# Optimization experiments

Measured on AMD Instinct MI355X. Metric: run time of the kernel, lower is better.

The kernel has to match this reference:

```python
import jax, jax.numpy as jnp
import numpy as np

NEG_SLOPE = 0.2
EPS = 1e-16


def gat_conv(x, src, dst, n_nodes, W, att_src, att_dst, b):
    """PyG GATConv, heads=1. x:[N,in], W:[out,in], att_*:[out], b:[out].
    Messages flow src->dst; softmax over incoming edges of each dst node."""
    h = x @ W.T                                  # [N, out]
    a_src = h @ att_src                          # [N]
    a_dst = h @ att_dst                          # [N]
    e = jax.nn.leaky_relu(a_src[src] + a_dst[dst], NEG_SLOPE)   # [E]
    m = jax.ops.segment_max(e, dst, num_segments=n_nodes)       # [N]
    ex = jnp.exp(e - m[dst])                                    # [E]
    denom = jax.ops.segment_sum(ex, dst, num_segments=n_nodes)  # [N]
    alpha = ex / (denom[dst] + EPS)                             # [E]
    out = jax.ops.segment_sum(h[src] * alpha[:, None], dst, num_segments=n_nodes)
    return out + b


def setup_inputs() -> dict:
    key = jax.random.key(0)
    ks = jax.random.split(key, 12)
    N, E = 100000, 1280000
    d_in, d_hid, d_out = 2, 64, 2

    def glorot(k, shape):
        fan = shape[-1] + shape[0]
        s = jnp.sqrt(6.0 / fan)
        return jax.random.uniform(k, shape, jnp.float32, -s, s)

    return {
        "x": jax.random.normal(ks[0], (N, d_in), jnp.float32),
        "edge_index": jax.random.randint(ks[1], (2, E), 0, N, jnp.int64)
            if jax.config.jax_enable_x64 else
            jax.random.randint(ks[1], (2, E), 0, N, jnp.int32),
        "W1": glorot(ks[2], (d_hid, d_in)),
        "att_src1": glorot(ks[3], (d_hid,)),
        "att_dst1": glorot(ks[4], (d_hid,)),
        "b1": jnp.zeros((d_hid,), jnp.float32),
        "W2": glorot(ks[5], (d_out, d_hid)),
        "att_src2": glorot(ks[6], (d_out,)),
        "att_dst2": glorot(ks[7], (d_out,)),
        "b2": jnp.zeros((d_out,), jnp.float32),
    }


def reference(x, edge_index, W1, att_src1, att_dst1, b1, W2, att_src2, att_dst2, b2):
    n_nodes = x.shape[0]
    # add self-loops (PyG GATConv default)
    loops = jnp.arange(n_nodes, dtype=edge_index.dtype)
    src = jnp.concatenate([edge_index[0], loops])
    dst = jnp.concatenate([edge_index[1], loops])

    h = gat_conv(x, src, dst, n_nodes, W1, att_src1, att_dst1, b1)
    h = jax.nn.relu(h)
    # dropout p=0.6 is identity in eval mode
    h = gat_conv(h, src, dst, n_nodes, W2, att_src2, att_dst2, b2)
    return jax.nn.log_softmax(h, axis=1)
```

## Files before the change

kernel.cpp:

```cpp
#include <hip/hip_runtime.h>
#include <cstdint>

#define NEG_SLOPE 0.2f
#define EPS 1e-16f
#define BSH 7
#define BNODES (1 << BSH)
#define NBMAX 1024
#define MAXDEG 64
#define ROWP 65
#define BKT_T 1024
#define BEPT 8
#define SEG 32
#define SEGSH 5
#define NBLK_MAX 512

__device__ __forceinline__ float lrelu(float x) {
    return (x >= 0.f) ? x : NEG_SLOPE * x;
}

template <int CTRL>
__device__ __forceinline__ float dpp_ror_add(float v) {
    int r = __builtin_amdgcn_update_dpp(0, __float_as_int(v), CTRL, 0xf, 0xf, true);
    return v + __int_as_float(r);
}
__device__ __forceinline__ float wave_sum(float v) {
    v = dpp_ror_add<0x121>(v);
    v = dpp_ror_add<0x122>(v);
    v = dpp_ror_add<0x124>(v);
    v = dpp_ror_add<0x128>(v);
    v += __shfl_xor(v, 16);
    v += __shfl_xor(v, 32);
    return v;
}

__global__ __launch_bounds__(BKT_T)
void bucket_kernel(const int* __restrict__ src, const int* __restrict__ dst,
                   unsigned* __restrict__ bkt, unsigned char* __restrict__ cntg,
                   int E, int nbuck, int nblk) {
    __shared__ int cnt[NBMAX];
    int tid = threadIdx.x, blk = blockIdx.x;
    cnt[tid] = 0;
    __syncthreads();
    long long blockBase = (long long)blk * (BKT_T * BEPT);
    int slots = nblk << SEGSH;
    #pragma unroll
    for (int k = 0; k < BEPT; ++k) {
        long long i = blockBase + k * BKT_T + tid;
        if (i < E) {
            int s = src[i], d = dst[i];
            int bk = d >> BSH;
            int r = atomicAdd(&cnt[bk], 1);
            if (r < SEG)
                bkt[(size_t)bk * slots + (blk << SEGSH) + r] =
                    ((unsigned)s << BSH) | (unsigned)(d & (BNODES - 1));
        }
    }
    __syncthreads();
    if (tid < nbuck) {
        int c = cnt[tid];
        if (c > SEG) c = SEG;
        cntg[(size_t)blk * NBMAX + tid] = (unsigned char)c;
    }
}

__global__ __launch_bounds__(128)
void agg1t_kernel(const unsigned char* __restrict__ cntg,
                  const unsigned* __restrict__ bkt,
                  const float2* __restrict__ x,
                  const float* __restrict__ W1, const float* __restrict__ as1,
                  const float* __restrict__ ad1, const float* __restrict__ b1,
                  const float* __restrict__ W2, const float* __restrict__ as2,
                  const float* __restrict__ ad2, float4* __restrict__ pack2,
                  int N, int nblk) {
    __shared__ int rows[BNODES * ROWP];
    __shared__ int cur[BNODES];
    __shared__ float4 tab[64];
    __shared__ float w2bL[64];
    __shared__ float4 cbox;
    __shared__ unsigned char cntL[NBLK_MAX];
    int b = blockIdx.x, tid = threadIdx.x;
    int nodeBase = b << BSH;
    cur[tid] = 0;
    if (tid < 64) {
        float w0 = W1[2 * tid], w1v = W1[2 * tid + 1];
        tab[tid] = make_float4(w0, w1v, b1[tid], W2[tid]);
        w2bL[tid] = W2[64 + tid];
        float s = as1[tid], d = ad1[tid];
        float c0 = wave_sum(w0 * s);
        float c1 = wave_sum(w1v * s);
        float e0 = wave_sum(w0 * d);
        float e1 = wave_sum(w1v * d);
        if (tid == 0) cbox = make_float4(c0, c1, e0, e1);
    }
    for (int s = tid; s < nblk; s += 128)
        cntL[s] = cntg[(size_t)s * NBMAX + b];
    __syncthreads();

    int slots = nblk << SEGSH;
    const unsigned* bp = bkt + (size_t)b * slots;
    for (int g = tid; g < slots; g += 128) {
        if ((g & (SEG - 1)) < (int)cntL[g >> SEGSH]) {
            unsigned p = bp[g];
            int ld = p & (BNODES - 1);
            int r = atomicAdd(&cur[ld], 1);
            if (r < MAXDEG) rows[ld * ROWP + r] = (int)(p >> BSH);
        }
    }
    __syncthreads();

    int i = tid;
    int n = nodeBase + i;
    if (n >= N) return;
    int dg = cur[i];
    if (dg > MAXDEG) dg = MAXDEG;
    float4 c = cbox;
    float2 xn = x[n];
    float asrc_n = fmaf(xn.x, c.x, xn.y * c.y);
    float adst_n = fmaf(xn.x, c.z, xn.y * c.w);

    float pvs = __expf(lrelu(asrc_n + adst_n));
    float sp = pvs, s0 = pvs * xn.x, s1 = pvs * xn.y;
    for (int r = 0; r < dg; ++r) {
        int s = rows[i * ROWP + r];
        float2 xs = x[s];
        float e = lrelu(fmaf(xs.x, c.x, xs.y * c.y) + adst_n);
        float pv = __expf(e);
        sp += pv;
        s0 = fmaf(pv, xs.x, s0);
        s1 = fmaf(pv, xs.y, s1);
    }
    float rden = 1.f / (sp + EPS);
    s0 *= rden;
    s1 *= rden;

    float q0 = 0.f, q1 = 0.f;
    #pragma unroll 8
    for (int j = 0; j < 64; ++j) {
        float4 t = tab[j];
        float hr = fmaxf(fmaf(t.x, s0, t.y * s1) + t.z, 0.f);
        q0 = fmaf(hr, t.w, q0);
        q1 = fmaf(hr, w2bL[j], q1);
    }
    float sa = as2[0], sb = as2[1], da = ad2[0], db = ad2[1];
    pack2[n] = make_float4(q0, q1,
                           fmaf(q0, sa, q1 * sb),
                           fmaf(q0, da, q1 * db));
}

__global__ __launch_bounds__(128)
void agg2t_kernel(const unsigned char* __restrict__ cntg,
                  const unsigned* __restrict__ bkt,
                  const float4* __restrict__ pack2, const float* __restrict__ b2,
                  float2* __restrict__ out, int N, int nblk) {
    __shared__ int rows[BNODES * ROWP];
    __shared__ int cur[BNODES];
    __shared__ unsigned char cntL[NBLK_MAX];
    int b = blockIdx.x, tid = threadIdx.x;
    int nodeBase = b << BSH;
    cur[tid] = 0;
    for (int s = tid; s < nblk; s += 128)
        cntL[s] = cntg[(size_t)s * NBMAX + b];
    __syncthreads();

    int slots = nblk << SEGSH;
    const unsigned* bp = bkt + (size_t)b * slots;
    for (int g = tid; g < slots; g += 128) {
        if ((g & (SEG - 1)) < (int)cntL[g >> SEGSH]) {
            unsigned p = bp[g];
            int ld = p & (BNODES - 1);
            int r = atomicAdd(&cur[ld], 1);
            if (r < MAXDEG) rows[ld * ROWP + r] = (int)(p >> BSH);
        }
    }
    __syncthreads();

    int i = tid;
    int n = nodeBase + i;
    if (n >= N) return;
    int dg = cur[i];
    if (dg > MAXDEG) dg = MAXDEG;
    float4 Pn = pack2[n];
    float adst_n = Pn.w;

    float pvs = __expf(lrelu(Pn.z + adst_n));
    float sp = pvs, a0 = pvs * Pn.x, a1 = pvs * Pn.y;
    for (int r = 0; r < dg; ++r) {
        int s = rows[i * ROWP + r];
        float4 P = pack2[s];
        float pv = __expf(lrelu(P.z + adst_n));
        sp += pv;
        a0 = fmaf(pv, P.x, a0);
        a1 = fmaf(pv, P.y, a1);
    }
    float rd = 1.f / (sp + EPS);
    float v0 = fmaf(a0, rd, b2[0]);
    float v1 = fmaf(a1, rd, b2[1]);
    float mx = fmaxf(v0, v1);
    float lse = mx + logf(__expf(v0 - mx) + __expf(v1 - mx));
    out[n] = make_float2(v0 - lse, v1 - lse);
}

extern "C" void kernel_launch(void* const* d_in, const int* in_sizes, int n_in,
                              void* d_out, int out_size, void* d_ws, size_t ws_size,
                              hipStream_t stream) {
    const float* x      = (const float*)d_in[0];
    const int*   eidx   = (const int*)d_in[1];
    const float* W1     = (const float*)d_in[2];
    const float* att_s1 = (const float*)d_in[3];
    const float* att_d1 = (const float*)d_in[4];
    const float* b1     = (const float*)d_in[5];
    const float* W2     = (const float*)d_in[6];
    const float* att_s2 = (const float*)d_in[7];
    const float* att_d2 = (const float*)d_in[8];
    const float* b2     = (const float*)d_in[9];

    const int N     = in_sizes[0] / 2;
    const int E     = in_sizes[1] / 2;
    const int nbuck = (N + BNODES - 1) >> BSH;
    const int nblk  = (E + BKT_T * BEPT - 1) / (BKT_T * BEPT);
    const int slots = nblk << SEGSH;

    const int* src = eidx;
    const int* dst = eidx + E;

    char* w = (char*)(((uintptr_t)d_ws + 15) & ~(uintptr_t)15);
    unsigned*      bkt  = (unsigned*)w;       w += (size_t)nbuck * slots * 4;
    unsigned char* cntg = (unsigned char*)w;  w += (size_t)nblk * NBMAX;
    w = (char*)(((uintptr_t)w + 15) & ~(uintptr_t)15);
    float4*        pack2 = (float4*)w;        w += (size_t)N * 16;

    bucket_kernel<<<dim3(nblk), dim3(BKT_T), 0, stream>>>(
        src, dst, bkt, cntg, E, nbuck, nblk);

    agg1t_kernel<<<dim3(nbuck), dim3(128), 0, stream>>>(
        cntg, bkt, (const float2*)x, W1, att_s1, att_d1, b1, W2, att_s2, att_d2,
        pack2, N, nblk);

    agg2t_kernel<<<dim3(nbuck), dim3(128), 0, stream>>>(
        cntg, bkt, pack2, b2, (float2*)d_out, N, nblk);
}
```

Before: 62.82 us.

## Replace fixed-slot edge buckets with per-block counting-sort regions and offsets

The bucket kernel now does two passes: it counts edges per destination bucket, runs a shared-memory prefix scan, then scatters packed edges into a compact per-block region sorted by bucket, and records start/count pairs. The aggregation kernels read each block's contiguous segment via those offsets instead of scanning fixed 32-slot padded segments. This removes the wasted reads of padded slots and the silent drop of edges beyond 32 per segment. In exchange the bucket kernel reads dst twice and does a 1024-wide log-step scan, and in the aggregation kernels each thread now walks one variable-length segment serially, which can be unbalanced across threads.

```diff
diff --git a/kernel.cpp b/kernel.cpp
--- a/kernel.cpp
+++ b/kernel.cpp
@@ -10,8 +10,7 @@
 #define ROWP 65
 #define BKT_T 1024
 #define BEPT 8
-#define SEG 32
-#define SEGSH 5
+#define BLKE (BKT_T * BEPT)
 #define NBLK_MAX 512
 
 __device__ __forceinline__ float lrelu(float x) {
@@ -35,36 +34,53 @@
 
 __global__ __launch_bounds__(BKT_T)
 void bucket_kernel(const int* __restrict__ src, const int* __restrict__ dst,
-                   unsigned* __restrict__ bkt, unsigned char* __restrict__ cntg,
-                   int E, int nbuck, int nblk) {
+                   unsigned* __restrict__ bkt, unsigned* __restrict__ offs,
+                   int E) {
     __shared__ int cnt[NBMAX];
+    __shared__ int pref[NBMAX];
     int tid = threadIdx.x, blk = blockIdx.x;
+    long long base = (long long)blk * BLKE;
     cnt[tid] = 0;
     __syncthreads();
-    long long blockBase = (long long)blk * (BKT_T * BEPT);
-    int slots = nblk << SEGSH;
+
     #pragma unroll
     for (int k = 0; k < BEPT; ++k) {
-        long long i = blockBase + k * BKT_T + tid;
+        long long i = base + k * BKT_T + tid;
+        if (i < E) atomicAdd(&cnt[dst[i] >> BSH], 1);
+    }
+    __syncthreads();
+
+    int c = cnt[tid];
+    pref[tid] = c;
+    __syncthreads();
+    #pragma unroll
+    for (int off = 1; off < NBMAX; off <<= 1) {
+        int t = (tid >= off) ? pref[tid - off] : 0;
+        __syncthreads();
+        pref[tid] += t;
+        __syncthreads();
+    }
+    int start = pref[tid] - c;
+    offs[(size_t)blk * NBMAX + tid] =
+        ((unsigned)start << 16) | (unsigned)c;
+    cnt[tid] = start;
+    __syncthreads();
+
+    unsigned* reg = bkt + (size_t)blk * BLKE;
+    #pragma unroll
+    for (int k = 0; k < BEPT; ++k) {
+        long long i = base + k * BKT_T + tid;
         if (i < E) {
             int s = src[i], d = dst[i];
             int bk = d >> BSH;
             int r = atomicAdd(&cnt[bk], 1);
-            if (r < SEG)
-                bkt[(size_t)bk * slots + (blk << SEGSH) + r] =
-                    ((unsigned)s << BSH) | (unsigned)(d & (BNODES - 1));
+            reg[r] = ((unsigned)s << BSH) | (unsigned)(d & (BNODES - 1));
         }
     }
-    __syncthreads();
-    if (tid < nbuck) {
-        int c = cnt[tid];
-        if (c > SEG) c = SEG;
-        cntg[(size_t)blk * NBMAX + tid] = (unsigned char)c;
-    }
 }
 
 __global__ __launch_bounds__(128)
-void agg1t_kernel(const unsigned char* __restrict__ cntg,
+void agg1t_kernel(const unsigned* __restrict__ offs,
                   const unsigned* __restrict__ bkt,
                   const float2* __restrict__ x,
                   const float* __restrict__ W1, const float* __restrict__ as1,
@@ -77,7 +93,7 @@
     __shared__ float4 tab[64];
     __shared__ float w2bL[64];
     __shared__ float4 cbox;
-    __shared__ unsigned char cntL[NBLK_MAX];
+    __shared__ unsigned offsL[NBLK_MAX];
     int b = blockIdx.x, tid = threadIdx.x;
     int nodeBase = b << BSH;
     cur[tid] = 0;
@@ -93,14 +109,15 @@
         if (tid == 0) cbox = make_float4(c0, c1, e0, e1);
     }
     for (int s = tid; s < nblk; s += 128)
-        cntL[s] = cntg[(size_t)s * NBMAX + b];
-    __syncthreads();
-
-    int slots = nblk << SEGSH;
-    const unsigned* bp = bkt + (size_t)b * slots;
-    for (int g = tid; g < slots; g += 128) {
-        if ((g & (SEG - 1)) < (int)cntL[g >> SEGSH]) {
-            unsigned p = bp[g];
+        offsL[s] = offs[(size_t)s * NBMAX + b];
+    __syncthreads();
+
+    for (int blkq = tid; blkq < nblk; blkq += 128) {
+        unsigned o = offsL[blkq];
+        int st = (int)(o >> 16), c = (int)(o & 0xFFFFu);
+        const unsigned* q = bkt + (size_t)blkq * BLKE + st;
+        for (int j = 0; j < c; ++j) {
+            unsigned p = q[j];
             int ld = p & (BNODES - 1);
             int r = atomicAdd(&cur[ld], 1);
             if (r < MAXDEG) rows[ld * ROWP + r] = (int)(p >> BSH);
@@ -148,25 +165,26 @@
 }
 
 __global__ __launch_bounds__(128)
-void agg2t_kernel(const unsigned char* __restrict__ cntg,
+void agg2t_kernel(const unsigned* __restrict__ offs,
                   const unsigned* __restrict__ bkt,
                   const float4* __restrict__ pack2, const float* __restrict__ b2,
                   float2* __restrict__ out, int N, int nblk) {
     __shared__ int rows[BNODES * ROWP];
     __shared__ int cur[BNODES];
-    __shared__ unsigned char cntL[NBLK_MAX];
+    __shared__ unsigned offsL[NBLK_MAX];
     int b = blockIdx.x, tid = threadIdx.x;
     int nodeBase = b << BSH;
     cur[tid] = 0;
     for (int s = tid; s < nblk; s += 128)
-        cntL[s] = cntg[(size_t)s * NBMAX + b];
-    __syncthreads();
-
-    int slots = nblk << SEGSH;
-    const unsigned* bp = bkt + (size_t)b * slots;
-    for (int g = tid; g < slots; g += 128) {
-        if ((g & (SEG - 1)) < (int)cntL[g >> SEGSH]) {
-            unsigned p = bp[g];
+        offsL[s] = offs[(size_t)s * NBMAX + b];
+    __syncthreads();
+
+    for (int blkq = tid; blkq < nblk; blkq += 128) {
+        unsigned o = offsL[blkq];
+        int st = (int)(o >> 16), c = (int)(o & 0xFFFFu);
+        const unsigned* q = bkt + (size_t)blkq * BLKE + st;
+        for (int j = 0; j < c; ++j) {
+            unsigned p = q[j];
             int ld = p & (BNODES - 1);
             int r = atomicAdd(&cur[ld], 1);
             if (r < MAXDEG) rows[ld * ROWP + r] = (int)(p >> BSH);
@@ -217,25 +235,22 @@
     const int N     = in_sizes[0] / 2;
     const int E     = in_sizes[1] / 2;
     const int nbuck = (N + BNODES - 1) >> BSH;
-    const int nblk  = (E + BKT_T * BEPT - 1) / (BKT_T * BEPT);
-    const int slots = nblk << SEGSH;
+    const int nblk  = (E + BLKE - 1) / BLKE;
 
     const int* src = eidx;
     const int* dst = eidx + E;
 
     char* w = (char*)(((uintptr_t)d_ws + 15) & ~(uintptr_t)15);
-    unsigned*      bkt  = (unsigned*)w;       w += (size_t)nbuck * slots * 4;
-    unsigned char* cntg = (unsigned char*)w;  w += (size_t)nblk * NBMAX;
-    w = (char*)(((uintptr_t)w + 15) & ~(uintptr_t)15);
-    float4*        pack2 = (float4*)w;        w += (size_t)N * 16;
-
-    bucket_kernel<<<dim3(nblk), dim3(BKT_T), 0, stream>>>(
-        src, dst, bkt, cntg, E, nbuck, nblk);
+    unsigned* bkt   = (unsigned*)w;  w += (size_t)nblk * BLKE * 4;
+    unsigned* offs  = (unsigned*)w;  w += (size_t)nblk * NBMAX * 4;
+    float4*   pack2 = (float4*)w;    w += (size_t)N * 16;
+
+    bucket_kernel<<<dim3(nblk), dim3(BKT_T), 0, stream>>>(src, dst, bkt, offs, E);
 
     agg1t_kernel<<<dim3(nbuck), dim3(128), 0, stream>>>(
-        cntg, bkt, (const float2*)x, W1, att_s1, att_d1, b1, W2, att_s2, att_d2,
+        offs, bkt, (const float2*)x, W1, att_s1, att_d1, b1, W2, att_s2, att_d2,
         pack2, N, nblk);
 
     agg2t_kernel<<<dim3(nbuck), dim3(128), 0, stream>>>(
-        cntg, bkt, pack2, b2, (float2*)d_out, N, nblk);
-}
+        offs, bkt, pack2, b2, (float2*)d_out, N, nblk);
+}
```

Result: slower. 66.28 us (+5.5%).
